# Optimization experiments

Hardware: AMD Instinct MI355X
Metric: run time of the kernel (lower is better)

## Reference

```python
import jax, jax.numpy as jnp
import numpy as np

# Dims: batch=64, n_cols=512, n_e=80, n_i=20, embed=512
DT_OVER_TAU = 0.1  # leaky rate-neuron integration constant (dt/tau)

B, C, NE, NI, E = 64, 512, 80, 20, 512


def setup_inputs() -> dict:
    key = jax.random.key(0)
    ks = jax.random.split(key, 12)
    return {
        "thal": jax.random.normal(ks[0], (B, E), jnp.float32),
        "thal_increments": jax.random.normal(ks[1], (B, C, E), jnp.float32),
        "l23_fb": jax.random.normal(ks[2], (B, C, NE), jnp.float32),
        # state (rates nonnegative, membrane potentials gaussian)
        "r_e": jax.random.uniform(ks[3], (B, C, NE), jnp.float32),
        "r_i": jax.random.uniform(ks[4], (B, C, NI), jnp.float32),
        "e_v": jax.random.normal(ks[5], (B, C, NE), jnp.float32),
        "i_v": jax.random.normal(ks[6], (B, C, NI), jnp.float32),
        # learned params (per-column weight stacks)
        "input_proj": jax.random.normal(ks[7], (C, NE, E), jnp.float32) * (1.0 / np.sqrt(E).astype(np.float32)),
        "feedback_proj": jax.random.normal(ks[8], (C, NE, NE), jnp.float32) * (1.0 / np.sqrt(NE).astype(np.float32)),
        # static synapses: nonnegative weights, sign handled by E/I convention
        "W_ee": jax.random.uniform(ks[9], (C, NE, NE), jnp.float32) * (1.0 / np.sqrt(NE).astype(np.float32)),
        "W_ei": jax.random.uniform(ks[10], (C, NI, NE), jnp.float32) * (1.0 / np.sqrt(NE).astype(np.float32)),
        "W_ie": jax.random.uniform(ks[11], (C, NE, NI), jnp.float32) * (1.0 / np.sqrt(NI).astype(np.float32)),
    }


def reference(thal, thal_increments, l23_fb, r_e, r_i, e_v, i_v,
              input_proj, feedback_proj, W_ee, W_ei, W_ie):
    # thal [B,E] broadcast over columns + per-column increments -> [B,C,E]
    thal_full = thal[:, None, :] + thal_increments
    # external + feedback drive onto excitatory pop: [B,C,NE]
    I_ext = jnp.einsum('bce,coe->bco', thal_full, input_proj)
    I_fb = jnp.einsum('bce,coe->bco', l23_fb, feedback_proj)
    # synapse currents (static weights; E->E, E->I excitatory, I->E inhibitory)
    I_ee = jnp.einsum('bcp,cop->bco', r_e, W_ee)   # [B,C,NE]
    I_ei = jnp.einsum('bcp,cop->bco', r_e, W_ei)   # [B,C,NI]
    I_ie = -jnp.einsum('bcp,cop->bco', r_i, W_ie)  # [B,C,NE], inhibitory
    I_e_total = I_ext + I_fb + I_ee + I_ie
    I_i_total = I_ei
    # leaky rate-neuron state update: v <- v + dt/tau * (-v + I); r = relu(v)
    v_e_new = e_v + DT_OVER_TAU * (I_e_total - e_v)
    v_i_new = i_v + DT_OVER_TAU * (I_i_total - i_v)
    r_e_new = jax.nn.relu(v_e_new)
    r_i_new = jax.nn.relu(v_i_new)
    # (layer_outputs e_out/l23_out/l5_out all alias r_e_new; return new state too)
    return r_e_new, r_i_new, v_e_new, v_i_new
```

## Files before the change

### kernel.cpp

```cpp
#include <hip/hip_runtime.h>
#include <hip/hip_bf16.h>

typedef __attribute__((ext_vector_type(8))) short bf16x8;
typedef __attribute__((ext_vector_type(4))) float f32x4;
typedef unsigned short u16;
typedef unsigned int u32;

__device__ __forceinline__ u16 f2bf(float f) {
  __hip_bfloat16 h = __float2bfloat16(f);
  u16 u;
  __builtin_memcpy(&u, &h, 2);
  return u;
}
__device__ __forceinline__ void cvt4_store(u16* dst, float4 v) {
  u16 rr[4] = {f2bf(v.x), f2bf(v.y), f2bf(v.z), f2bf(v.w)};
  uint2 p;
  __builtin_memcpy(&p, rr, 8);
  *(uint2*)dst = p;
}


__global__ __launch_bounds__(256) void ei_cols_mfma(
    const float* __restrict__ thal,
    const float* __restrict__ inc,
    const float* __restrict__ l23,
    const float* __restrict__ re_in,
    const float* __restrict__ ri_in,
    const float* __restrict__ ev_in,
    const float* __restrict__ iv_in,
    const float* __restrict__ in_proj,
    const float* __restrict__ fb_proj,
    const float* __restrict__ w_ee,
    const float* __restrict__ w_ei,
    const float* __restrict__ w_ie,
    float* __restrict__ out)
{
  __shared__ __align__(16) unsigned char smem[41472];
  const int c = blockIdx.x;
  const int tid = threadIdx.x;
  const int lane = tid & 63;
  const int wave = tid >> 6;
  const int nidx = lane & 15;
  const int quad = lane >> 4;
  const int m0 = wave * 16;

  f32x4 acc_e[5], acc_i[2];
#pragma unroll
  for (int j = 0; j < 5; ++j) acc_e[j] = (f32x4){0.f, 0.f, 0.f, 0.f};
#pragma unroll
  for (int j = 0; j < 2; ++j) acc_i[j] = (f32x4){0.f, 0.f, 0.f, 0.f};

  {
    float4 tv[4], gv[4], wv[5];

    auto load_regs = [&](int k0) {
#pragma unroll
      for (int j = 0; j < 4; ++j) {
        int l = tid + j * 256;
        int b = l >> 4, kk = (l & 15) << 2;
        tv[j] = *(const float4*)(thal + b * 512 + k0 + kk);
        gv[j] = *(const float4*)(inc + (size_t)b * 262144 + (size_t)c * 512 + k0 + kk);
      }
#pragma unroll
      for (int j = 0; j < 5; ++j) {
        int l = tid + j * 256;
        int o = l >> 4, kk = (l & 15) << 2;
        wv[j] = *(const float4*)(in_proj + (size_t)c * 40960 + o * 512 + k0 + kk);
      }
    };
    auto store_buf = [&](int p) {
      u16* A = (u16*)(smem + p * 20736);
      u16* W = (u16*)(smem + 9216 + p * 20736);
#pragma unroll
      for (int j = 0; j < 4; ++j) {
        int l = tid + j * 256;
        int b = l >> 4, kk = (l & 15) << 2;
        float4 s;
        s.x = tv[j].x + gv[j].x; s.y = tv[j].y + gv[j].y;
        s.z = tv[j].z + gv[j].z; s.w = tv[j].w + gv[j].w;
        cvt4_store(A + b * 72 + kk, s);
      }
#pragma unroll
      for (int j = 0; j < 5; ++j) {
        int l = tid + j * 256;
        int o = l >> 4, kk = (l & 15) << 2;
        cvt4_store(W + o * 72 + kk, wv[j]);
      }
    };

    load_regs(0);
    store_buf(0);
    for (int i = 0; i < 8; ++i) {
      __syncthreads();
      if (i < 7) load_regs((i + 1) * 64);
      const int p = i & 1;
      u16* A = (u16*)(smem + p * 20736);
      u16* W = (u16*)(smem + 9216 + p * 20736);
#pragma unroll
      for (int kk0 = 0; kk0 < 64; kk0 += 32) {
        bf16x8 a = *(const bf16x8*)(A + (m0 + nidx) * 72 + kk0 + quad * 8);
#pragma unroll
        for (int j = 0; j < 5; ++j) {
          bf16x8 b = *(const bf16x8*)(W + (j * 16 + nidx) * 72 + kk0 + quad * 8);
          acc_e[j] = __builtin_amdgcn_mfma_f32_16x16x32_bf16(a, b, acc_e[j], 0, 0, 0);
        }
      }
      if (i < 7) store_buf((i + 1) & 1);
    }
  }

  {
    __syncthreads();
    u16* As = (u16*)smem;
    u16* Bs = (u16*)(smem + 13312);
    for (int l = tid; l < 1280; l += 256) {
      int b = l / 20, kk = (l % 20) << 2;
      cvt4_store(As + b * 104 + kk,
                 *(const float4*)(l23 + ((size_t)b * 512 + c) * 80 + kk));
    }
    for (int l = tid; l < 128; l += 256) {
      int b = l >> 1, off = 80 + (l & 1) * 8;
      *(uint4*)(As + b * 104 + off) = (uint4){0u, 0u, 0u, 0u};
    }
    for (int l = tid; l < 1600; l += 256) {
      int o = l / 20, kk = (l % 20) << 2;
      cvt4_store(Bs + o * 104 + kk,
                 *(const float4*)(fb_proj + ((size_t)c * 80 + o) * 80 + kk));
    }
    for (int l = tid; l < 160; l += 256) {
      int o = l >> 1, off = 80 + (l & 1) * 8;
      *(uint4*)(Bs + o * 104 + off) = (uint4){0u, 0u, 0u, 0u};
    }
    __syncthreads();
#pragma unroll
    for (int kk0 = 0; kk0 < 96; kk0 += 32) {
      bf16x8 a = *(const bf16x8*)(As + (m0 + nidx) * 104 + kk0 + quad * 8);
#pragma unroll
      for (int j = 0; j < 5; ++j) {
        bf16x8 b = *(const bf16x8*)(Bs + (j * 16 + nidx) * 104 + kk0 + quad * 8);
        acc_e[j] = __builtin_amdgcn_mfma_f32_16x16x32_bf16(a, b, acc_e[j], 0, 0, 0);
      }
    }
  }

  {
    __syncthreads();
    u16* As = (u16*)smem;
    u16* W1 = (u16*)(smem + 13312);
    u16* W2 = (u16*)(smem + 29952);
    for (int l = tid; l < 1280; l += 256) {
      int b = l / 20, kk = (l % 20) << 2;
      cvt4_store(As + b * 104 + kk,
                 *(const float4*)(re_in + ((size_t)b * 512 + c) * 80 + kk));
    }
    for (int l = tid; l < 128; l += 256) {
      int b = l >> 1, off = 80 + (l & 1) * 8;
      *(uint4*)(As + b * 104 + off) = (uint4){0u, 0u, 0u, 0u};
    }
    for (int l = tid; l < 1600; l += 256) {
      int o = l / 20, kk = (l % 20) << 2;
      cvt4_store(W1 + o * 104 + kk,
                 *(const float4*)(w_ee + ((size_t)c * 80 + o) * 80 + kk));
    }
    for (int l = tid; l < 160; l += 256) {
      int o = l >> 1, off = 80 + (l & 1) * 8;
      *(uint4*)(W1 + o * 104 + off) = (uint4){0u, 0u, 0u, 0u};
    }
    for (int l = tid; l < 400; l += 256) {
      int o = l / 20, kk = (l % 20) << 2;
      cvt4_store(W2 + o * 104 + kk,
                 *(const float4*)(w_ei + ((size_t)c * 20 + o) * 80 + kk));
    }
    for (int l = tid; l < 40; l += 256) {
      int o = l >> 1, off = 80 + (l & 1) * 8;
      *(uint4*)(W2 + o * 104 + off) = (uint4){0u, 0u, 0u, 0u};
    }
    for (int l = tid; l < 156; l += 256) {
      int o = 20 + l / 13, off = (l % 13) * 8;
      *(uint4*)(W2 + o * 104 + off) = (uint4){0u, 0u, 0u, 0u};
    }
    __syncthreads();
#pragma unroll
    for (int kk0 = 0; kk0 < 96; kk0 += 32) {
      bf16x8 a = *(const bf16x8*)(As + (m0 + nidx) * 104 + kk0 + quad * 8);
#pragma unroll
      for (int j = 0; j < 5; ++j) {
        bf16x8 b = *(const bf16x8*)(W1 + (j * 16 + nidx) * 104 + kk0 + quad * 8);
        acc_e[j] = __builtin_amdgcn_mfma_f32_16x16x32_bf16(a, b, acc_e[j], 0, 0, 0);
      }
#pragma unroll
      for (int j = 0; j < 2; ++j) {
        bf16x8 b = *(const bf16x8*)(W2 + (j * 16 + nidx) * 104 + kk0 + quad * 8);
        acc_i[j] = __builtin_amdgcn_mfma_f32_16x16x32_bf16(a, b, acc_i[j], 0, 0, 0);
      }
    }
  }

  {
    __syncthreads();
    u16* Ri = (u16*)smem;
    u16* Wn = (u16*)(smem + 5120);
    for (int l = tid; l < 320; l += 256) {
      int b = l / 5, kk = (l % 5) << 2;
      cvt4_store(Ri + b * 40 + kk,
                 *(const float4*)(ri_in + ((size_t)b * 512 + c) * 20 + kk));
    }
    for (int l = tid; l < 192; l += 256) {
      int b = l / 3, kk = 20 + (l % 3) * 4;
      *(uint2*)(Ri + b * 40 + kk) = (uint2){0u, 0u};
    }
    for (int l = tid; l < 400; l += 256) {
      int o = l / 5, kk = (l % 5) << 2;
      float4 v = *(const float4*)(w_ie + ((size_t)c * 80 + o) * 20 + kk);
      v.x = -v.x; v.y = -v.y; v.z = -v.z; v.w = -v.w;
      cvt4_store(Wn + o * 40 + kk, v);
    }
    for (int l = tid; l < 240; l += 256) {
      int o = l / 3, kk = 20 + (l % 3) * 4;
      *(uint2*)(Wn + o * 40 + kk) = (uint2){0u, 0u};
    }
    __syncthreads();
    {
      bf16x8 a = *(const bf16x8*)(Ri + (m0 + nidx) * 40 + quad * 8);
#pragma unroll
      for (int j = 0; j < 5; ++j) {
        bf16x8 b = *(const bf16x8*)(Wn + (j * 16 + nidx) * 40 + quad * 8);
        acc_e[j] = __builtin_amdgcn_mfma_f32_16x16x32_bf16(a, b, acc_e[j], 0, 0, 0);
      }
    }
  }

  __syncthreads();
  float* aE = (float*)smem;
  float* aI = (float*)(smem + 21504);
#pragma unroll
  for (int j = 0; j < 5; ++j)
#pragma unroll
    for (int r = 0; r < 4; ++r)
      aE[(m0 + quad * 4 + r) * 84 + j * 16 + nidx] = acc_e[j][r];
#pragma unroll
  for (int j = 0; j < 2; ++j) {
    int col = j * 16 + nidx;
    if (col < 20) {
#pragma unroll
      for (int r = 0; r < 4; ++r)
        aI[(m0 + quad * 4 + r) * 36 + col] = acc_i[j][r];
    }
  }
  __syncthreads();

  const size_t R_ri = 2621440u;
  const size_t R_ve = 3276800u;
  const size_t R_vi = 5898240u;
  for (int l = tid; l < 1280; l += 256) {
    int b = l / 20, c2 = (l % 20) << 2;
    float4 a = *(const float4*)(aE + b * 84 + c2);
    size_t g = ((size_t)b * 512 + c) * 80 + c2;
    float4 ev = *(const float4*)(ev_in + g);
    float4 v, r;
    v.x = ev.x + 0.1f * (a.x - ev.x); r.x = fmaxf(v.x, 0.f);
    v.y = ev.y + 0.1f * (a.y - ev.y); r.y = fmaxf(v.y, 0.f);
    v.z = ev.z + 0.1f * (a.z - ev.z); r.z = fmaxf(v.z, 0.f);
    v.w = ev.w + 0.1f * (a.w - ev.w); r.w = fmaxf(v.w, 0.f);
    *(float4*)(out + g) = r;
    *(float4*)(out + R_ve + g) = v;
  }
  for (int l = tid; l < 320; l += 256) {
    int b = l / 5, c2 = (l % 5) << 2;
    float4 a = *(const float4*)(aI + b * 36 + c2);
    size_t g = ((size_t)b * 512 + c) * 20 + c2;
    float4 iv = *(const float4*)(iv_in + g);
    float4 v, r;
    v.x = iv.x + 0.1f * (a.x - iv.x); r.x = fmaxf(v.x, 0.f);
    v.y = iv.y + 0.1f * (a.y - iv.y); r.y = fmaxf(v.y, 0.f);
    v.z = iv.z + 0.1f * (a.z - iv.z); r.z = fmaxf(v.z, 0.f);
    v.w = iv.w + 0.1f * (a.w - iv.w); r.w = fmaxf(v.w, 0.f);
    *(float4*)(out + R_ri + g) = r;
    *(float4*)(out + R_vi + g) = v;
  }
}

extern "C" void kernel_launch(void* const* d_in, const int* in_sizes, int n_in,
                              void* d_out, int out_size, void* d_ws, size_t ws_size,
                              hipStream_t stream) {
  const float* thal = (const float*)d_in[0];
  const float* inc = (const float*)d_in[1];
  const float* l23 = (const float*)d_in[2];
  const float* re = (const float*)d_in[3];
  const float* ri = (const float*)d_in[4];
  const float* ev = (const float*)d_in[5];
  const float* iv = (const float*)d_in[6];
  const float* in_proj = (const float*)d_in[7];
  const float* fb_proj = (const float*)d_in[8];
  const float* w_ee = (const float*)d_in[9];
  const float* w_ei = (const float*)d_in[10];
  const float* w_ie = (const float*)d_in[11];
  float* out = (float*)d_out;
  ei_cols_mfma<<<dim3(512), dim3(256), 0, stream>>>(
      thal, inc, l23, re, ri, ev, iv, in_proj, fb_proj, w_ee, w_ei, w_ie, out);
}
```

Baseline: 257.9 us.

## Split batch across two blocks per column and partition N tiles across waves

Result: no change. 260.2 us (+0.9%).

```diff
diff --git a/kernel.cpp b/kernel.cpp
--- a/kernel.cpp
+++ b/kernel.cpp
@@ -1,5 +1,4 @@
 #include <hip/hip_runtime.h>
-#include <hip/hip_bf16.h>
 
 typedef __attribute__((ext_vector_type(8))) short bf16x8;
 typedef __attribute__((ext_vector_type(4))) float f32x4;
@@ -7,10 +6,10 @@
 typedef unsigned int u32;
 
 __device__ __forceinline__ u16 f2bf(float f) {
-  __hip_bfloat16 h = __float2bfloat16(f);
-  u16 u;
-  __builtin_memcpy(&u, &h, 2);
-  return u;
+  u32 x;
+  __builtin_memcpy(&x, &f, 4);
+  u32 r = x + 0x7fffu + ((x >> 16) & 1u);
+  return (u16)(r >> 16);
 }
 __device__ __forceinline__ void cvt4_store(u16* dst, float4 v) {
   u16 rr[4] = {f2bf(v.x), f2bf(v.y), f2bf(v.z), f2bf(v.w)};
@@ -20,7 +19,7 @@
 }
 
 
-__global__ __launch_bounds__(256) void ei_cols_mfma(
+__global__ __launch_bounds__(256, 4) void ei_cols_mfma(
     const float* __restrict__ thal,
     const float* __restrict__ inc,
     const float* __restrict__ l23,
@@ -35,31 +34,36 @@
     const float* __restrict__ w_ie,
     float* __restrict__ out)
 {
-  __shared__ __align__(16) unsigned char smem[41472];
-  const int c = blockIdx.x;
+  __shared__ __align__(16) unsigned char smem[32256];
+  const int c = blockIdx.x >> 1;
+  const int bh = blockIdx.x & 1;
+  const size_t bbase = (size_t)bh * 32;
   const int tid = threadIdx.x;
   const int lane = tid & 63;
   const int wave = tid >> 6;
   const int nidx = lane & 15;
   const int quad = lane >> 4;
-  const int m0 = wave * 16;
-
-  f32x4 acc_e[5], acc_i[2];
-#pragma unroll
-  for (int j = 0; j < 5; ++j) acc_e[j] = (f32x4){0.f, 0.f, 0.f, 0.f};
+  const int t = wave >> 1;
+  const int par = wave & 1;
+  const int m0 = t * 16;
+  const int ne0 = par ? 3 : 0;
+  const int nE = par ? 2 : 3;
+
+  f32x4 acc_e[3], acc_i[2];
+#pragma unroll
+  for (int j = 0; j < 3; ++j) acc_e[j] = (f32x4){0.f, 0.f, 0.f, 0.f};
 #pragma unroll
   for (int j = 0; j < 2; ++j) acc_i[j] = (f32x4){0.f, 0.f, 0.f, 0.f};
 
   {
-    float4 tv[4], gv[4], wv[5];
-
+    float4 tv[2], gv[2], wv[5];
     auto load_regs = [&](int k0) {
 #pragma unroll
-      for (int j = 0; j < 4; ++j) {
+      for (int j = 0; j < 2; ++j) {
         int l = tid + j * 256;
         int b = l >> 4, kk = (l & 15) << 2;
-        tv[j] = *(const float4*)(thal + b * 512 + k0 + kk);
-        gv[j] = *(const float4*)(inc + (size_t)b * 262144 + (size_t)c * 512 + k0 + kk);
+        tv[j] = *(const float4*)(thal + (bbase + b) * 512 + k0 + kk);
+        gv[j] = *(const float4*)(inc + (bbase + b) * 262144 + (size_t)c * 512 + k0 + kk);
       }
 #pragma unroll
       for (int j = 0; j < 5; ++j) {
@@ -69,10 +73,10 @@
       }
     };
     auto store_buf = [&](int p) {
-      u16* A = (u16*)(smem + p * 20736);
-      u16* W = (u16*)(smem + 9216 + p * 20736);
-#pragma unroll
-      for (int j = 0; j < 4; ++j) {
+      u16* A = (u16*)(smem + p * 16128);
+      u16* W = (u16*)(smem + 4608 + p * 16128);
+#pragma unroll
+      for (int j = 0; j < 2; ++j) {
         int l = tid + j * 256;
         int b = l >> 4, kk = (l & 15) << 2;
         float4 s;
@@ -94,15 +98,17 @@
       __syncthreads();
       if (i < 7) load_regs((i + 1) * 64);
       const int p = i & 1;
-      u16* A = (u16*)(smem + p * 20736);
-      u16* W = (u16*)(smem + 9216 + p * 20736);
+      const u16* A = (const u16*)(smem + p * 16128);
+      const u16* W = (const u16*)(smem + 4608 + p * 16128);
 #pragma unroll
       for (int kk0 = 0; kk0 < 64; kk0 += 32) {
         bf16x8 a = *(const bf16x8*)(A + (m0 + nidx) * 72 + kk0 + quad * 8);
 #pragma unroll
-        for (int j = 0; j < 5; ++j) {
-          bf16x8 b = *(const bf16x8*)(W + (j * 16 + nidx) * 72 + kk0 + quad * 8);
-          acc_e[j] = __builtin_amdgcn_mfma_f32_16x16x32_bf16(a, b, acc_e[j], 0, 0, 0);
+        for (int j = 0; j < 3; ++j) {
+          if (j < nE) {
+            bf16x8 b = *(const bf16x8*)(W + ((ne0 + j) * 16 + nidx) * 72 + kk0 + quad * 8);
+            acc_e[j] = __builtin_amdgcn_mfma_f32_16x16x32_bf16(a, b, acc_e[j], 0, 0, 0);
+          }
         }
       }
       if (i < 7) store_buf((i + 1) & 1);
@@ -112,33 +118,35 @@
   {
     __syncthreads();
     u16* As = (u16*)smem;
-    u16* Bs = (u16*)(smem + 13312);
-    for (int l = tid; l < 1280; l += 256) {
+    u16* Bs = (u16*)(smem + 6656);
+    for (int l = tid; l < 640; l += 256) {
       int b = l / 20, kk = (l % 20) << 2;
       cvt4_store(As + b * 104 + kk,
-                 *(const float4*)(l23 + ((size_t)b * 512 + c) * 80 + kk));
-    }
-    for (int l = tid; l < 128; l += 256) {
-      int b = l >> 1, off = 80 + (l & 1) * 8;
-      *(uint4*)(As + b * 104 + off) = (uint4){0u, 0u, 0u, 0u};
+                 *(const float4*)(l23 + ((bbase + b) * 512 + c) * 80 + kk));
+    }
+    for (int l = tid; l < 96; l += 256) {
+      int b = l / 3, s = l % 3;
+      *(uint4*)(As + b * 104 + 80 + s * 8) = (uint4){0u, 0u, 0u, 0u};
     }
     for (int l = tid; l < 1600; l += 256) {
       int o = l / 20, kk = (l % 20) << 2;
       cvt4_store(Bs + o * 104 + kk,
                  *(const float4*)(fb_proj + ((size_t)c * 80 + o) * 80 + kk));
     }
-    for (int l = tid; l < 160; l += 256) {
-      int o = l >> 1, off = 80 + (l & 1) * 8;
-      *(uint4*)(Bs + o * 104 + off) = (uint4){0u, 0u, 0u, 0u};
+    for (int l = tid; l < 240; l += 256) {
+      int o = l / 3, s = l % 3;
+      *(uint4*)(Bs + o * 104 + 80 + s * 8) = (uint4){0u, 0u, 0u, 0u};
     }
     __syncthreads();
 #pragma unroll
     for (int kk0 = 0; kk0 < 96; kk0 += 32) {
       bf16x8 a = *(const bf16x8*)(As + (m0 + nidx) * 104 + kk0 + quad * 8);
 #pragma unroll
-      for (int j = 0; j < 5; ++j) {
-        bf16x8 b = *(const bf16x8*)(Bs + (j * 16 + nidx) * 104 + kk0 + quad * 8);
-        acc_e[j] = __builtin_amdgcn_mfma_f32_16x16x32_bf16(a, b, acc_e[j], 0, 0, 0);
+      for (int j = 0; j < 3; ++j) {
+        if (j < nE) {
+          bf16x8 b = *(const bf16x8*)(Bs + ((ne0 + j) * 16 + nidx) * 104 + kk0 + quad * 8);
+          acc_e[j] = __builtin_amdgcn_mfma_f32_16x16x32_bf16(a, b, acc_e[j], 0, 0, 0);
+        }
       }
     }
   }
@@ -146,52 +154,56 @@
   {
     __syncthreads();
     u16* As = (u16*)smem;
-    u16* W1 = (u16*)(smem + 13312);
-    u16* W2 = (u16*)(smem + 29952);
-    for (int l = tid; l < 1280; l += 256) {
+    u16* W1 = (u16*)(smem + 6656);
+    u16* W2 = (u16*)(smem + 23296);
+    for (int l = tid; l < 640; l += 256) {
       int b = l / 20, kk = (l % 20) << 2;
       cvt4_store(As + b * 104 + kk,
-                 *(const float4*)(re_in + ((size_t)b * 512 + c) * 80 + kk));
-    }
-    for (int l = tid; l < 128; l += 256) {
-      int b = l >> 1, off = 80 + (l & 1) * 8;
-      *(uint4*)(As + b * 104 + off) = (uint4){0u, 0u, 0u, 0u};
+                 *(const float4*)(re_in + ((bbase + b) * 512 + c) * 80 + kk));
+    }
+    for (int l = tid; l < 96; l += 256) {
+      int b = l / 3, s = l % 3;
+      *(uint4*)(As + b * 104 + 80 + s * 8) = (uint4){0u, 0u, 0u, 0u};
     }
     for (int l = tid; l < 1600; l += 256) {
       int o = l / 20, kk = (l % 20) << 2;
       cvt4_store(W1 + o * 104 + kk,
                  *(const float4*)(w_ee + ((size_t)c * 80 + o) * 80 + kk));
     }
-    for (int l = tid; l < 160; l += 256) {
-      int o = l >> 1, off = 80 + (l & 1) * 8;
-      *(uint4*)(W1 + o * 104 + off) = (uint4){0u, 0u, 0u, 0u};
+    for (int l = tid; l < 240; l += 256) {
+      int o = l / 3, s = l % 3;
+      *(uint4*)(W1 + o * 104 + 80 + s * 8) = (uint4){0u, 0u, 0u, 0u};
     }
     for (int l = tid; l < 400; l += 256) {
       int o = l / 20, kk = (l % 20) << 2;
       cvt4_store(W2 + o * 104 + kk,
                  *(const float4*)(w_ei + ((size_t)c * 20 + o) * 80 + kk));
     }
-    for (int l = tid; l < 40; l += 256) {
-      int o = l >> 1, off = 80 + (l & 1) * 8;
-      *(uint4*)(W2 + o * 104 + off) = (uint4){0u, 0u, 0u, 0u};
+    for (int l = tid; l < 60; l += 256) {
+      int o = l / 3, s = l % 3;
+      *(uint4*)(W2 + o * 104 + 80 + s * 8) = (uint4){0u, 0u, 0u, 0u};
     }
     for (int l = tid; l < 156; l += 256) {
-      int o = 20 + l / 13, off = (l % 13) * 8;
-      *(uint4*)(W2 + o * 104 + off) = (uint4){0u, 0u, 0u, 0u};
+      int o = 20 + l / 13, s = l % 13;
+      *(uint4*)(W2 + o * 104 + s * 8) = (uint4){0u, 0u, 0u, 0u};
     }
     __syncthreads();
 #pragma unroll
     for (int kk0 = 0; kk0 < 96; kk0 += 32) {
       bf16x8 a = *(const bf16x8*)(As + (m0 + nidx) * 104 + kk0 + quad * 8);
 #pragma unroll
-      for (int j = 0; j < 5; ++j) {
-        bf16x8 b = *(const bf16x8*)(W1 + (j * 16 + nidx) * 104 + kk0 + quad * 8);
-        acc_e[j] = __builtin_amdgcn_mfma_f32_16x16x32_bf16(a, b, acc_e[j], 0, 0, 0);
-      }
-#pragma unroll
-      for (int j = 0; j < 2; ++j) {
-        bf16x8 b = *(const bf16x8*)(W2 + (j * 16 + nidx) * 104 + kk0 + quad * 8);
-        acc_i[j] = __builtin_amdgcn_mfma_f32_16x16x32_bf16(a, b, acc_i[j], 0, 0, 0);
+      for (int j = 0; j < 3; ++j) {
+        if (j < nE) {
+          bf16x8 b = *(const bf16x8*)(W1 + ((ne0 + j) * 16 + nidx) * 104 + kk0 + quad * 8);
+          acc_e[j] = __builtin_amdgcn_mfma_f32_16x16x32_bf16(a, b, acc_e[j], 0, 0, 0);
+        }
+      }
+      if (par) {
+#pragma unroll
+        for (int j = 0; j < 2; ++j) {
+          bf16x8 b = *(const bf16x8*)(W2 + (j * 16 + nidx) * 104 + kk0 + quad * 8);
+          acc_i[j] = __builtin_amdgcn_mfma_f32_16x16x32_bf16(a, b, acc_i[j], 0, 0, 0);
+        }
       }
     }
   }
@@ -199,15 +211,15 @@
   {
     __syncthreads();
     u16* Ri = (u16*)smem;
-    u16* Wn = (u16*)(smem + 5120);
-    for (int l = tid; l < 320; l += 256) {
+    u16* Wn = (u16*)(smem + 2560);
+    for (int l = tid; l < 160; l += 256) {
       int b = l / 5, kk = (l % 5) << 2;
       cvt4_store(Ri + b * 40 + kk,
-                 *(const float4*)(ri_in + ((size_t)b * 512 + c) * 20 + kk));
-    }
-    for (int l = tid; l < 192; l += 256) {
-      int b = l / 3, kk = 20 + (l % 3) * 4;
-      *(uint2*)(Ri + b * 40 + kk) = (uint2){0u, 0u};
+                 *(const float4*)(ri_in + ((bbase + b) * 512 + c) * 20 + kk));
+    }
+    for (int l = tid; l < 96; l += 256) {
+      int b = l / 3, s = l % 3;
+      *(uint2*)(Ri + b * 40 + 20 + s * 4) = (uint2){0u, 0u};
     }
     for (int l = tid; l < 400; l += 256) {
       int o = l / 5, kk = (l % 5) << 2;
@@ -216,35 +228,42 @@
       cvt4_store(Wn + o * 40 + kk, v);
     }
     for (int l = tid; l < 240; l += 256) {
-      int o = l / 3, kk = 20 + (l % 3) * 4;
-      *(uint2*)(Wn + o * 40 + kk) = (uint2){0u, 0u};
+      int o = l / 3, s = l % 3;
+      *(uint2*)(Wn + o * 40 + 20 + s * 4) = (uint2){0u, 0u};
     }
     __syncthreads();
     {
       bf16x8 a = *(const bf16x8*)(Ri + (m0 + nidx) * 40 + quad * 8);
 #pragma unroll
-      for (int j = 0; j < 5; ++j) {
-        bf16x8 b = *(const bf16x8*)(Wn + (j * 16 + nidx) * 40 + quad * 8);
-        acc_e[j] = __builtin_amdgcn_mfma_f32_16x16x32_bf16(a, b, acc_e[j], 0, 0, 0);
+      for (int j = 0; j < 3; ++j) {
+        if (j < nE) {
+          bf16x8 b = *(const bf16x8*)(Wn + ((ne0 + j) * 16 + nidx) * 40 + quad * 8);
+          acc_e[j] = __builtin_amdgcn_mfma_f32_16x16x32_bf16(a, b, acc_e[j], 0, 0, 0);
+        }
       }
     }
   }
 
   __syncthreads();
   float* aE = (float*)smem;
-  float* aI = (float*)(smem + 21504);
-#pragma unroll
-  for (int j = 0; j < 5; ++j)
-#pragma unroll
-    for (int r = 0; r < 4; ++r)
-      aE[(m0 + quad * 4 + r) * 84 + j * 16 + nidx] = acc_e[j][r];
-#pragma unroll
-  for (int j = 0; j < 2; ++j) {
-    int col = j * 16 + nidx;
-    if (col < 20) {
+  float* aI = (float*)(smem + 10752);
+#pragma unroll
+  for (int j = 0; j < 3; ++j) {
+    if (j < nE) {
 #pragma unroll
       for (int r = 0; r < 4; ++r)
-        aI[(m0 + quad * 4 + r) * 36 + col] = acc_i[j][r];
+        aE[(m0 + quad * 4 + r) * 84 + (ne0 + j) * 16 + nidx] = acc_e[j][r];
+    }
+  }
+  if (par) {
+#pragma unroll
+    for (int j = 0; j < 2; ++j) {
+      int col = j * 16 + nidx;
+      if (col < 20) {
+#pragma unroll
+        for (int r = 0; r < 4; ++r)
+          aI[(m0 + quad * 4 + r) * 36 + col] = acc_i[j][r];
+      }
     }
   }
   __syncthreads();
@@ -252,10 +271,10 @@
   const size_t R_ri = 2621440u;
   const size_t R_ve = 3276800u;
   const size_t R_vi = 5898240u;
-  for (int l = tid; l < 1280; l += 256) {
+  for (int l = tid; l < 640; l += 256) {
     int b = l / 20, c2 = (l % 20) << 2;
     float4 a = *(const float4*)(aE + b * 84 + c2);
-    size_t g = ((size_t)b * 512 + c) * 80 + c2;
+    size_t g = ((bbase + b) * 512 + c) * 80 + c2;
     float4 ev = *(const float4*)(ev_in + g);
     float4 v, r;
     v.x = ev.x + 0.1f * (a.x - ev.x); r.x = fmaxf(v.x, 0.f);
@@ -265,10 +284,10 @@
     *(float4*)(out + g) = r;
     *(float4*)(out + R_ve + g) = v;
   }
-  for (int l = tid; l < 320; l += 256) {
+  for (int l = tid; l < 160; l += 256) {
     int b = l / 5, c2 = (l % 5) << 2;
     float4 a = *(const float4*)(aI + b * 36 + c2);
-    size_t g = ((size_t)b * 512 + c) * 20 + c2;
+    size_t g = ((bbase + b) * 512 + c) * 20 + c2;
     float4 iv = *(const float4*)(iv_in + g);
     float4 v, r;
     v.x = iv.x + 0.1f * (a.x - iv.x); r.x = fmaxf(v.x, 0.f);
@@ -296,6 +315,6 @@
   const float* w_ei = (const float*)d_in[10];
   const float* w_ie = (const float*)d_in[11];
   float* out = (float*)d_out;
-  ei_cols_mfma<<<dim3(512), dim3(256), 0, stream>>>(
+  ei_cols_mfma<<<dim3(1024), dim3(256), 0, stream>>>(
       thal, inc, l23, re, ri, ev, iv, in_proj, fb_proj, w_ee, w_ei, w_ie, out);
 }
```
